# Optimization experiments

Hardware: AMD Instinct MI355X
Metric: run time of the kernel (lower is better)

The kernel has to match this reference:

```python
import jax, jax.numpy as jnp
import numpy as np

B, L, D = 16, 1024, 512
MAX_LEN = 1024  # module hardcodes self.max_len = 1024


def setup_inputs() -> dict:
    key = jax.random.key(0)
    k0, k1, k2, k3, k4 = jax.random.split(key, 5)
    s = 1.0 / np.sqrt(D)
    return {
        "x": jax.random.normal(k0, (B, L, D), jnp.float32),
        "generator": 0.02 * jax.random.normal(k1, (D, 2 * MAX_LEN - 1), jnp.float32),
        "Wq": jax.random.normal(k2, (D, D), jnp.float32) * s,
        "Wv": jax.random.normal(k3, (D, D), jnp.float32) * s,
        "Wc": jax.random.normal(k4, (D, D), jnp.float32) * s,
    }


def reference(x, generator, Wq, Wv, Wc):
    Bc, Lc, Dc = x.shape
    q = x @ Wq.T                      # (B, L, D)
    v = x @ Wv.T                      # (B, L, D)
    # extract_center_window: window of size 2L-1 centered at MAX_LEN-1
    center_full = (generator.shape[-1] + 1) // 2  # == MAX_LEN
    gen = generator[:, center_full - Lc: center_full + Lc - 1]  # (D, 2L-1)
    w = jnp.einsum('bld,di->bli', q, gen)  # (B, L, 2L-1)
    # Toeplitz gather: out[b, l, i] = w[b, l, (L-1) - l + i]
    r = jnp.arange(Lc)
    idx = (Lc - 1) - r[:, None] + r[None, :]  # (L, L)
    w = jnp.take_along_axis(w, idx[None, :, :], axis=-1)  # (B, L, L)
    w = jnp.cumsum(w, axis=1)
    w = jax.nn.relu(w)
    w = jnp.tril(w)
    w = w / (jnp.sum(w, axis=-1, keepdims=True) + 1e-8)
    out = jnp.einsum('bli,bid->bld', w, v)  # (B, L, D)
    return out @ Wc.T
```

## Files before the change

### kernel.cpp

```cpp
#include <hip/hip_runtime.h>
#include <hip/hip_bf16.h>

typedef __attribute__((ext_vector_type(8))) __bf16 bf16x8;
typedef __attribute__((ext_vector_type(4))) __bf16 bf16x4;
typedef __attribute__((ext_vector_type(4))) float  f32x4;

__device__ __forceinline__ void gl_lds16(const __bf16* g, __bf16* l) {
  __builtin_amdgcn_global_load_lds(
      (const __attribute__((address_space(1))) void*)g,
      (__attribute__((address_space(3))) void*)l,
      16, 0, 0);
}

__global__ __launch_bounds__(256) void prep_kernel(
    const float* __restrict__ x, const float* __restrict__ gen,
    const float* __restrict__ Wq, const float* __restrict__ Wv, const float* __restrict__ Wc,
    __bf16* __restrict__ xb, __bf16* __restrict__ genT,
    __bf16* __restrict__ wqT, __bf16* __restrict__ wvT, __bf16* __restrict__ wcb,
    float* __restrict__ gp) {
  __shared__ float S[64][65];
  const int blk = blockIdx.x, tid = threadIdx.x;

  if (blk < 128) {
    const float* in = (blk < 64) ? Wq : Wv;
    __bf16* out = (blk < 64) ? wqT : wvT;
    int t = blk & 63;
    int tx = tid & 63, ty = tid >> 6;
    int d0 = (t >> 3) * 64, e0 = (t & 7) * 64;
#pragma unroll
    for (int i = 0; i < 16; ++i) {
      int di = i * 4 + ty;
      S[di][tx] = in[(long)(d0 + di) * 512 + e0 + tx];
    }
    __syncthreads();
#pragma unroll
    for (int i = 0; i < 16; ++i) {
      int ei = i * 4 + ty;
      out[(long)(e0 + ei) * 512 + d0 + tx] = (__bf16)S[tx][ei];
    }
  } else if (blk < 384) {
    int i = (blk - 128) * 256 + tid;
    float4 v = ((const float4*)Wc)[i];
    bf16x4 o;
    o[0] = (__bf16)v.x; o[1] = (__bf16)v.y; o[2] = (__bf16)v.z; o[3] = (__bf16)v.w;
    *(bf16x4*)(wcb + 4L * i) = o;
  } else if (blk < 2432) {
    int i = blk - 384;
    for (int d = tid; d < 512; d += 256) {
      float v = (i < 2047) ? gen[(long)d * 2047 + i] : 0.f;
      genT[(long)i * 512 + d] = (__bf16)v;
    }
  } else if (blk < 10624) {
    int i = (blk - 2432) * 256 + tid;
    float4 v = ((const float4*)x)[i];
    bf16x4 o;
    o[0] = (__bf16)v.x; o[1] = (__bf16)v.y; o[2] = (__bf16)v.z; o[3] = (__bf16)v.w;
    *(bf16x4*)(xb + 4L * i) = o;
  } else {
    int t = blk - 10624;
    int i = t % 63, c = t / 63;
    int d0 = c * 64, k = tid;
    float a0 = 0.f, a1 = 0.f;
#pragma unroll 8
    for (int u = 0; u < 64; ++u) {
      int d = d0 + u;
      float g = gen[(long)d * 2047 + 992 + i];
      a0 += Wq[(long)d * 512 + k] * g;
      a1 += Wq[(long)d * 512 + k + 256] * g;
    }
    long o = ((long)c * 63 + i) * 512;
    gp[o + k] = a0;
    gp[o + k + 256] = a1;
  }
}

__global__ void g2t_reduce(const float* __restrict__ gp, float* __restrict__ g2t) {
  int idx = blockIdx.x * 256 + threadIdx.x;
  if (idx >= 63 * 512) return;
  float s = 0.f;
#pragma unroll
  for (int c = 0; c < 8; ++c) s += gp[(long)c * 63 * 512 + idx];
  g2t[idx] = s;
}

template <int MODE, bool TRIL = false>
__global__ __launch_bounds__(256) void gemm_bt(
    const __bf16* __restrict__ A, const __bf16* __restrict__ B, void* __restrict__ Cv,
    const float* __restrict__ aux, int N, int K, long sA, long sB, long sC, int sAux) {
  __shared__ __bf16 As[2][128 * 32];
  __shared__ __bf16 Bs[2][128 * 32];
  const int tid = threadIdx.x;
  const int w = tid >> 6, l = tid & 63;
  const int m0 = blockIdx.y * 128;
  const int n0 = blockIdx.x * 128;
  const int bz = blockIdx.z;
  const __bf16* Ab = A + (long)bz * sA;
  const __bf16* Bb = B + (long)bz * sB;

  const int srow = w * 16 + (l >> 2);
  const int scol = (l & 3) * 8;
  const int wr = (w >> 1) * 64, wc = (w & 1) * 64;
  const int fr = l & 15, fk = (l >> 4) * 8;

  f32x4 acc[4][4] = {};

  const int KM = TRIL ? min(K, m0 + 128) : K;
  const int nt = KM >> 5;

  auto STAGE = [&](int t, int p) {
    const int k0 = t << 5;
    gl_lds16(Ab + (long)(m0 + srow) * K + (k0 + scol),      &As[p][(w * 16) * 32]);
    gl_lds16(Ab + (long)(m0 + 64 + srow) * K + (k0 + scol), &As[p][(64 + w * 16) * 32]);
    gl_lds16(Bb + (long)(n0 + srow) * K + (k0 + scol),      &Bs[p][(w * 16) * 32]);
    gl_lds16(Bb + (long)(n0 + 64 + srow) * K + (k0 + scol), &Bs[p][(64 + w * 16) * 32]);
  };

  STAGE(0, 0);
  STAGE(1, 1);

  for (int t = 0; t < nt; ++t) {
    if (t == nt - 1) asm volatile("s_waitcnt vmcnt(0)\ns_barrier" ::: "memory");
    else             asm volatile("s_waitcnt vmcnt(4)\ns_barrier" ::: "memory");
    const int p = t & 1;
    bf16x8 af[4], bg[4];
#pragma unroll
    for (int i = 0; i < 4; ++i) af[i] = *(const bf16x8*)&As[p][(wr + i * 16 + fr) * 32 + fk];
#pragma unroll
    for (int j = 0; j < 4; ++j) bg[j] = *(const bf16x8*)&Bs[p][(wc + j * 16 + fr) * 32 + fk];
    asm volatile("s_waitcnt lgkmcnt(0)\ns_barrier" ::: "memory");
    if (t + 2 < nt) STAGE(t + 2, p);
#pragma unroll
    for (int i = 0; i < 4; ++i)
#pragma unroll
      for (int j = 0; j < 4; ++j)
        acc[i][j] = __builtin_amdgcn_mfma_f32_16x16x32_bf16(af[i], bg[j], acc[i][j], 0, 0, 0);
  }

  const int rbase = m0 + wr + ((l >> 4) << 2);
  const int cbase = n0 + wc + fr;

  if constexpr (MODE == 1) {
    __bf16* C = (__bf16*)Cv + (long)bz * sC;
#pragma unroll
    for (int i = 0; i < 4; ++i)
#pragma unroll
      for (int r = 0; r < 4; ++r) {
        long row = rbase + i * 16 + r;
#pragma unroll
        for (int j = 0; j < 4; ++j) C[row * N + cbase + j * 16] = (__bf16)acc[i][j][r];
      }
  } else {
    float* C = (float*)Cv + (long)bz * sC;
    const float* ax = aux + (long)bz * sAux;
#pragma unroll
    for (int i = 0; i < 4; ++i)
#pragma unroll
      for (int r = 0; r < 4; ++r) {
        long row = rbase + i * 16 + r;
        float sc = 1.f / (ax[row] + 1e-8f);
#pragma unroll
        for (int j = 0; j < 4; ++j) C[row * N + cbase + j * 16] = acc[i][j][r] * sc;
      }
  }
}

__global__ __launch_bounds__(512) void gemm_x(
    const __bf16* __restrict__ A, const __bf16* __restrict__ Bg,
    const __bf16* __restrict__ Pm, __bf16* __restrict__ S, __bf16* __restrict__ vT) {
  __shared__ __bf16 As[2][256 * 32];
  __shared__ __bf16 Bs[2][128 * 32];
  const int tid = threadIdx.x;
  const int w = tid >> 6, l = tid & 63;

  int wgid = blockIdx.x;
  int swz = (wgid & 7) * 112 + (wgid >> 3);
  int y = swz / 14, xt = swz - y * 14;
  const bool band = (xt < 10);
  const int m0 = y * 256;
  const int n0 = band ? (6 - 2 * (y & 3) + xt) * 128 : (xt - 10) * 128;
  const __bf16* Bb = band ? Bg : Pm;
  const int K = 512;

  const int srow = w * 16 + (l >> 2);
  const int scol = (l & 3) * 8;
  const int wr = (w >> 1) * 64;
  const int wc = (w & 1) * 64;
  const int fr = l & 15, fk = (l >> 4) * 8;

  f32x4 acc[4][4] = {};

  auto STAGE = [&](int t, int p) {
    const int k0 = t << 5;
    gl_lds16(A + (long)(m0 + srow) * K + (k0 + scol),        &As[p][(w * 16) * 32]);
    gl_lds16(A + (long)(m0 + 128 + srow) * K + (k0 + scol),  &As[p][(128 + w * 16) * 32]);
    gl_lds16(Bb + (long)(n0 + srow) * K + (k0 + scol),       &Bs[p][(w * 16) * 32]);
  };

  STAGE(0, 0);
  STAGE(1, 1);

  for (int t = 0; t < 16; ++t) {
    if (t == 15) asm volatile("s_waitcnt vmcnt(0)\ns_barrier" ::: "memory");
    else         asm volatile("s_waitcnt vmcnt(3)\ns_barrier" ::: "memory");
    const int p = t & 1;
    bf16x8 af[4], bg[4];
#pragma unroll
    for (int i = 0; i < 4; ++i) af[i] = *(const bf16x8*)&As[p][(wr + i * 16 + fr) * 32 + fk];
#pragma unroll
    for (int j = 0; j < 4; ++j) bg[j] = *(const bf16x8*)&Bs[p][(wc + j * 16 + fr) * 32 + fk];
    asm volatile("s_waitcnt lgkmcnt(0)\ns_barrier" ::: "memory");
    if (t + 2 < 16) STAGE(t + 2, p);
#pragma unroll
    for (int i = 0; i < 4; ++i)
#pragma unroll
      for (int j = 0; j < 4; ++j)
        acc[i][j] = __builtin_amdgcn_mfma_f32_16x16x32_bf16(af[i], bg[j], acc[i][j], 0, 0, 0);
  }

  const int rbase = m0 + wr + ((l >> 4) << 2);
  const int cbase = n0 + wc + fr;

  if (band) {
#pragma unroll
    for (int i = 0; i < 4; ++i)
#pragma unroll
      for (int r = 0; r < 4; ++r) {
        int row = rbase + i * 16 + r;
        int lloc = row & 1023;
#pragma unroll
        for (int j = 0; j < 4; ++j) {
          int jj = cbase + j * 16 - 1023 + lloc;
          if ((unsigned)jj < 1024u)
            S[(long)row * 1024 + jj] = (__bf16)acc[i][j][r];
        }
      }
  } else {
#pragma unroll
    for (int i = 0; i < 4; ++i) {
      int gm = rbase + i * 16;
      int bt = gm >> 10, lloc = gm & 1023;
#pragma unroll
      for (int j = 0; j < 4; ++j) {
        bf16x4 pk;
        pk[0] = (__bf16)acc[i][j][0]; pk[1] = (__bf16)acc[i][j][1];
        pk[2] = (__bf16)acc[i][j][2]; pk[3] = (__bf16)acc[i][j][3];
        *(bf16x4*)&vT[((long)bt * 512 + cbase + j * 16) * 1024 + lloc] = pk;
      }
    }
  }
}

__global__ __launch_bounds__(128) void chunk_sums(const __bf16* __restrict__ S,
                                                  float* __restrict__ csum) {
  int j0 = threadIdx.x * 8;
  int c = blockIdx.x, b = blockIdx.y;
  const __bf16* Sb = S + (long)b * 1024 * 1024;
  float a[8] = {};
  int l0 = c * 16;
  for (int l = l0; l < l0 + 16; ++l) {
    bf16x8 v = *(const bf16x8*)&Sb[(long)l * 1024 + j0];
#pragma unroll
    for (int k = 0; k < 8; ++k) a[k] += (float)v[k];
  }
  long o = ((long)(b * 64 + c) << 10) + j0;
#pragma unroll
  for (int k = 0; k < 8; ++k) csum[o + k] = a[k];
}

__global__ void scan_kernel(float* __restrict__ csum) {
  int idx = blockIdx.x * 256 + threadIdx.x;
  int b = idx >> 10, j = idx & 1023;
  long base = ((long)b * 64 << 10) + j;
  float s = 0.f;
  for (int c = 0; c < 64; ++c) {
    long o = base + ((long)c << 10);
    float t = csum[o];
    csum[o] = s;
    s += t;
  }
}

__global__ __launch_bounds__(128) void cumsum_relu(const __bf16* __restrict__ S,
                                                   const float* __restrict__ csum,
                                                   __bf16* __restrict__ wrelu,
                                                   float* __restrict__ rowsum) {
  int j0 = threadIdx.x * 8;
  int c = blockIdx.x, b = blockIdx.y;
  float run[8];
  long co = ((long)(b * 64 + c) << 10) + j0;
#pragma unroll
  for (int k = 0; k < 8; ++k) run[k] = csum[co + k];
  const __bf16* Sb = S + (long)b * 1024 * 1024;
  __bf16* wr = wrelu + (long)b * 1024 * 1024;
  int l0 = c * 16;
  for (int l = l0; l < l0 + 16; ++l) {
    bf16x8 v = *(const bf16x8*)&Sb[(long)l * 1024 + j0];
    bf16x8 o;
    float rs = 0.f;
#pragma unroll
    for (int k = 0; k < 8; ++k) {
      run[k] += (float)v[k];
      float val = (j0 + k <= l) ? fmaxf(run[k], 0.f) : 0.f;
      o[k] = (__bf16)val;
      rs += val;
    }
    *(bf16x8*)&wr[(long)l * 1024 + j0] = o;
#pragma unroll
    for (int off = 32; off; off >>= 1) rs += __shfl_down(rs, off);
    if ((threadIdx.x & 63) == 0 && rs != 0.f) atomicAdd(&rowsum[b * 1024 + l], rs);
  }
}

__global__ __launch_bounds__(256) void small_dots(
    const float* __restrict__ x, const float* __restrict__ g2t, float* __restrict__ S) {
  int gid = blockIdx.x * 4 + (threadIdx.x >> 6);
  int lane = threadIdx.x & 63;
  int b = gid >> 10, rem = gid & 1023, m = rem >> 5, j = rem & 31;
  const float4* xr = (const float4*)(x + ((long)b * 1024 + m) * 512);
  const float4* gr = (const float4*)(g2t + (long)(31 - m + j) * 512);
  float4 a0 = xr[lane * 2], a1 = xr[lane * 2 + 1];
  float4 c0 = gr[lane * 2], c1 = gr[lane * 2 + 1];
  float s = a0.x * c0.x + a0.y * c0.y + a0.z * c0.z + a0.w * c0.w
          + a1.x * c1.x + a1.y * c1.y + a1.z * c1.z + a1.w * c1.w;
#pragma unroll
  for (int off = 32; off; off >>= 1) s += __shfl_down(s, off);
  if (lane == 0) S[gid] = s;
}

__global__ __launch_bounds__(1024) void small_scan(
    const float* __restrict__ Sg, __bf16* __restrict__ wrelu, float* __restrict__ rowsum) {
  int b = blockIdx.x, tid = threadIdx.x;
  __shared__ float S[32][33];
  int m = tid >> 5, j = tid & 31;
  S[m][j] = Sg[b * 1024 + tid];
  __syncthreads();
  if (tid < 32) {
    float run = 0.f;
    for (int mm = 0; mm < 32; ++mm) { run += S[mm][tid]; S[mm][tid] = run; }
  }
  __syncthreads();
  float v = (j <= m) ? fmaxf(S[m][j], 0.f) : 0.f;
  wrelu[((long)b * 1024 + m) * 1024 + j] = (__bf16)v;
  float rs = v;
#pragma unroll
  for (int off = 16; off; off >>= 1) rs += __shfl_down(rs, off, 32);
  if (j == 0) rowsum[b * 1024 + m] = rs;
}

extern "C" void kernel_launch(void* const* d_in, const int* in_sizes, int n_in,
                              void* d_out, int out_size, void* d_ws, size_t ws_size,
                              hipStream_t stream) {
  const float* x   = (const float*)d_in[0];
  const float* gen = (const float*)d_in[1];
  const float* Wq  = (const float*)d_in[2];
  const float* Wv  = (const float*)d_in[3];
  const float* Wc  = (const float*)d_in[4];

  char* ws = (char*)d_ws;
  __bf16* xb    = (__bf16*)(ws + 0L);
  __bf16* vT    = (__bf16*)(ws + 33554432L);
  __bf16* Smat  = (__bf16*)(ws + 67108864L);
  __bf16* wrelu = (__bf16*)(ws + 134217728L);
  __bf16* genT  = (__bf16*)(ws + 167772160L);
  __bf16* wqT   = (__bf16*)(ws + 169869312L);
  __bf16* wvT   = (__bf16*)(ws + 170393600L);
  __bf16* wcb   = (__bf16*)(ws + 170917888L);
  float*  g2t   = (float*)(ws + 171442176L);
  float*  csum  = (float*)(ws + 16777216L);
  float*  rsum  = (float*)(ws + 16777216L + 4194304L);
  float*  Sbuf  = (float*)(ws + 16777216L + 4259840L);
  __bf16* Pmat  = (__bf16*)(ws + 50331648L);
  __bf16* Bg    = (__bf16*)(ws + 51380224L);
  float*  gp    = (float*)(ws + 58720256L);

  prep_kernel<<<11128, 256, 0, stream>>>(x, gen, Wq, Wv, Wc, xb, genT, wqT, wvT, wcb, gp);
  g2t_reduce<<<126, 256, 0, stream>>>(gp, g2t);

  gemm_bt<1><<<dim3(4, 4, 1), 256, 0, stream>>>(wcb, wvT, Pmat, nullptr, 512, 512, 0, 0, 0, 0);
  gemm_bt<1><<<dim3(4, 16, 1), 256, 0, stream>>>(genT, wqT, Bg, nullptr, 512, 512, 0, 0, 0, 0);

  gemm_x<<<896, 512, 0, stream>>>(xb, Bg, Pmat, Smat, vT);

  chunk_sums<<<dim3(64, 16), 128, 0, stream>>>(Smat, csum);
  scan_kernel<<<64, 256, 0, stream>>>(csum);
  hipMemsetAsync(rsum, 0, 16 * 1024 * 4, stream);
  cumsum_relu<<<dim3(64, 16), 128, 0, stream>>>(Smat, csum, wrelu, rsum);

  small_dots<<<4096, 256, 0, stream>>>(x, g2t, Sbuf);
  small_scan<<<16, 1024, 0, stream>>>(Sbuf, wrelu, rsum);

  gemm_bt<4, true><<<dim3(4, 8, 16), 256, 0, stream>>>(wrelu, vT, d_out, rsum, 512, 1024,
                                                 1024L * 1024, 512L * 1024, 512L * 1024, 1024);
}
```

Baseline: 158.1 us.

## Triple-buffer GEMM pipelines, merge weight-fold GEMMs, drop memset and dead-tile writes

Moves the shared GEMM mainloop and gemm_x from double to triple LDS buffering with three tiles in flight, to hide more global-load latency. The two small weight-folding GEMMs become one 80-block launch, and the rowsum memset moves into chunk_sums, saving launches. cumsum_relu now skips writing wrelu tiles above the 128-block diagonal, which the tril-limited output GEMM never reads. Triple buffering raises LDS use per block, which may lower occupancy.

```diff
diff --git a/kernel.cpp b/kernel.cpp
--- a/kernel.cpp
+++ b/kernel.cpp
@@ -83,29 +83,15 @@
   g2t[idx] = s;
 }
 
-template <int MODE, bool TRIL = false>
-__global__ __launch_bounds__(256) void gemm_bt(
-    const __bf16* __restrict__ A, const __bf16* __restrict__ B, void* __restrict__ Cv,
-    const float* __restrict__ aux, int N, int K, long sA, long sB, long sC, int sAux) {
-  __shared__ __bf16 As[2][128 * 32];
-  __shared__ __bf16 Bs[2][128 * 32];
+__device__ __forceinline__ void gemm128_body(
+    const __bf16* __restrict__ Ab, const __bf16* __restrict__ Bb,
+    __bf16 (*As)[128 * 32], __bf16 (*Bs)[128 * 32],
+    int m0, int n0, int K, int nt, f32x4 (&acc)[4][4]) {
   const int tid = threadIdx.x;
   const int w = tid >> 6, l = tid & 63;
-  const int m0 = blockIdx.y * 128;
-  const int n0 = blockIdx.x * 128;
-  const int bz = blockIdx.z;
-  const __bf16* Ab = A + (long)bz * sA;
-  const __bf16* Bb = B + (long)bz * sB;
-
-  const int srow = w * 16 + (l >> 2);
-  const int scol = (l & 3) * 8;
+  const int srow = w * 16 + (l >> 2), scol = (l & 3) * 8;
   const int wr = (w >> 1) * 64, wc = (w & 1) * 64;
   const int fr = l & 15, fk = (l >> 4) * 8;
-
-  f32x4 acc[4][4] = {};
-
-  const int KM = TRIL ? min(K, m0 + 128) : K;
-  const int nt = KM >> 5;
 
   auto STAGE = [&](int t, int p) {
     const int k0 = t << 5;
@@ -114,61 +100,92 @@
     gl_lds16(Bb + (long)(n0 + srow) * K + (k0 + scol),      &Bs[p][(w * 16) * 32]);
     gl_lds16(Bb + (long)(n0 + 64 + srow) * K + (k0 + scol), &Bs[p][(64 + w * 16) * 32]);
   };
-
   STAGE(0, 0);
-  STAGE(1, 1);
-
+  if (nt > 1) STAGE(1, 1);
+  if (nt > 2) STAGE(2, 2);
+  int p = 0;
   for (int t = 0; t < nt; ++t) {
-    if (t == nt - 1) asm volatile("s_waitcnt vmcnt(0)\ns_barrier" ::: "memory");
-    else             asm volatile("s_waitcnt vmcnt(4)\ns_barrier" ::: "memory");
-    const int p = t & 1;
+    const int ahead = nt - 1 - t;
+    if (ahead >= 2)      asm volatile("s_waitcnt vmcnt(8)\ns_barrier" ::: "memory");
+    else if (ahead == 1) asm volatile("s_waitcnt vmcnt(4)\ns_barrier" ::: "memory");
+    else                 asm volatile("s_waitcnt vmcnt(0)\ns_barrier" ::: "memory");
     bf16x8 af[4], bg[4];
 #pragma unroll
     for (int i = 0; i < 4; ++i) af[i] = *(const bf16x8*)&As[p][(wr + i * 16 + fr) * 32 + fk];
 #pragma unroll
     for (int j = 0; j < 4; ++j) bg[j] = *(const bf16x8*)&Bs[p][(wc + j * 16 + fr) * 32 + fk];
     asm volatile("s_waitcnt lgkmcnt(0)\ns_barrier" ::: "memory");
-    if (t + 2 < nt) STAGE(t + 2, p);
+    if (t + 3 < nt) STAGE(t + 3, p);
 #pragma unroll
     for (int i = 0; i < 4; ++i)
 #pragma unroll
       for (int j = 0; j < 4; ++j)
         acc[i][j] = __builtin_amdgcn_mfma_f32_16x16x32_bf16(af[i], bg[j], acc[i][j], 0, 0, 0);
-  }
-
-  const int rbase = m0 + wr + ((l >> 4) << 2);
-  const int cbase = n0 + wc + fr;
-
-  if constexpr (MODE == 1) {
-    __bf16* C = (__bf16*)Cv + (long)bz * sC;
-#pragma unroll
-    for (int i = 0; i < 4; ++i)
-#pragma unroll
-      for (int r = 0; r < 4; ++r) {
-        long row = rbase + i * 16 + r;
-#pragma unroll
-        for (int j = 0; j < 4; ++j) C[row * N + cbase + j * 16] = (__bf16)acc[i][j][r];
-      }
-  } else {
-    float* C = (float*)Cv + (long)bz * sC;
-    const float* ax = aux + (long)bz * sAux;
-#pragma unroll
-    for (int i = 0; i < 4; ++i)
-#pragma unroll
-      for (int r = 0; r < 4; ++r) {
-        long row = rbase + i * 16 + r;
-        float sc = 1.f / (ax[row] + 1e-8f);
-#pragma unroll
-        for (int j = 0; j < 4; ++j) C[row * N + cbase + j * 16] = acc[i][j][r] * sc;
-      }
-  }
+    p = (p == 2) ? 0 : p + 1;
+  }
+}
+
+__global__ __launch_bounds__(256) void gemm_fold(
+    const __bf16* __restrict__ A1, const __bf16* __restrict__ B1, __bf16* __restrict__ C1,
+    const __bf16* __restrict__ A2, const __bf16* __restrict__ B2, __bf16* __restrict__ C2) {
+  __shared__ __bf16 As[3][128 * 32];
+  __shared__ __bf16 Bs[3][128 * 32];
+  const int b = blockIdx.x;
+  const __bf16 *Ab, *Bb; __bf16* C; int m0, n0;
+  if (b < 16) { Ab = A1; Bb = B1; C = C1; m0 = (b >> 2) * 128; n0 = (b & 3) * 128; }
+  else { int t = b - 16; Ab = A2; Bb = B2; C = C2; m0 = (t >> 2) * 128; n0 = (t & 3) * 128; }
+
+  f32x4 acc[4][4] = {};
+  gemm128_body(Ab, Bb, As, Bs, m0, n0, 512, 16, acc);
+
+  const int l = threadIdx.x & 63, w = threadIdx.x >> 6;
+  const int rbase = m0 + (w >> 1) * 64 + ((l >> 4) << 2);
+  const int cbase = n0 + (w & 1) * 64 + (l & 15);
+#pragma unroll
+  for (int i = 0; i < 4; ++i)
+#pragma unroll
+    for (int r = 0; r < 4; ++r) {
+      long row = rbase + i * 16 + r;
+#pragma unroll
+      for (int j = 0; j < 4; ++j) C[row * 512 + cbase + j * 16] = (__bf16)acc[i][j][r];
+    }
+}
+
+__global__ __launch_bounds__(256) void gemm_out(
+    const __bf16* __restrict__ A, const __bf16* __restrict__ B, float* __restrict__ Cv,
+    const float* __restrict__ aux) {
+  __shared__ __bf16 As[3][128 * 32];
+  __shared__ __bf16 Bs[3][128 * 32];
+  const int m0 = blockIdx.y * 128, n0 = blockIdx.x * 128, bz = blockIdx.z;
+  const int K = 1024;
+  const __bf16* Ab = A + (long)bz * 1024 * 1024;
+  const __bf16* Bb = B + (long)bz * 512 * 1024;
+  const int nt = (m0 + 128) >> 5;
+
+  f32x4 acc[4][4] = {};
+  gemm128_body(Ab, Bb, As, Bs, m0, n0, K, nt, acc);
+
+  const int l = threadIdx.x & 63, w = threadIdx.x >> 6;
+  const int rbase = m0 + (w >> 1) * 64 + ((l >> 4) << 2);
+  const int cbase = n0 + (w & 1) * 64 + (l & 15);
+  float* C = Cv + (long)bz * 512 * 1024;
+  const float* ax = aux + bz * 1024;
+#pragma unroll
+  for (int i = 0; i < 4; ++i)
+#pragma unroll
+    for (int r = 0; r < 4; ++r) {
+      long row = rbase + i * 16 + r;
+      float sc = 1.f / (ax[row] + 1e-8f);
+#pragma unroll
+      for (int j = 0; j < 4; ++j) C[row * 512 + cbase + j * 16] = acc[i][j][r] * sc;
+    }
 }
 
 __global__ __launch_bounds__(512) void gemm_x(
     const __bf16* __restrict__ A, const __bf16* __restrict__ Bg,
     const __bf16* __restrict__ Pm, __bf16* __restrict__ S, __bf16* __restrict__ vT) {
-  __shared__ __bf16 As[2][256 * 32];
-  __shared__ __bf16 Bs[2][128 * 32];
+  __shared__ __bf16 As[3][256 * 32];
+  __shared__ __bf16 Bs[3][128 * 32];
   const int tid = threadIdx.x;
   const int w = tid >> 6, l = tid & 63;
 
@@ -198,23 +215,27 @@
 
   STAGE(0, 0);
   STAGE(1, 1);
-
+  STAGE(2, 2);
+
+  int p = 0;
   for (int t = 0; t < 16; ++t) {
-    if (t == 15) asm volatile("s_waitcnt vmcnt(0)\ns_barrier" ::: "memory");
-    else         asm volatile("s_waitcnt vmcnt(3)\ns_barrier" ::: "memory");
-    const int p = t & 1;
+    const int ahead = 15 - t;
+    if (ahead >= 2)      asm volatile("s_waitcnt vmcnt(6)\ns_barrier" ::: "memory");
+    else if (ahead == 1) asm volatile("s_waitcnt vmcnt(3)\ns_barrier" ::: "memory");
+    else                 asm volatile("s_waitcnt vmcnt(0)\ns_barrier" ::: "memory");
     bf16x8 af[4], bg[4];
 #pragma unroll
     for (int i = 0; i < 4; ++i) af[i] = *(const bf16x8*)&As[p][(wr + i * 16 + fr) * 32 + fk];
 #pragma unroll
     for (int j = 0; j < 4; ++j) bg[j] = *(const bf16x8*)&Bs[p][(wc + j * 16 + fr) * 32 + fk];
     asm volatile("s_waitcnt lgkmcnt(0)\ns_barrier" ::: "memory");
-    if (t + 2 < 16) STAGE(t + 2, p);
+    if (t + 3 < 16) STAGE(t + 3, p);
 #pragma unroll
     for (int i = 0; i < 4; ++i)
 #pragma unroll
       for (int j = 0; j < 4; ++j)
         acc[i][j] = __builtin_amdgcn_mfma_f32_16x16x32_bf16(af[i], bg[j], acc[i][j], 0, 0, 0);
+    p = (p == 2) ? 0 : p + 1;
   }
 
   const int rbase = m0 + wr + ((l >> 4) << 2);
@@ -251,9 +272,11 @@
 }
 
 __global__ __launch_bounds__(128) void chunk_sums(const __bf16* __restrict__ S,
-                                                  float* __restrict__ csum) {
+                                                  float* __restrict__ csum,
+                                                  float* __restrict__ rowsum) {
   int j0 = threadIdx.x * 8;
   int c = blockIdx.x, b = blockIdx.y;
+  if (c < 8) rowsum[b * 1024 + c * 128 + threadIdx.x] = 0.f;
   const __bf16* Sb = S + (long)b * 1024 * 1024;
   float a[8] = {};
   int l0 = c * 16;
@@ -304,7 +327,8 @@
       o[k] = (__bf16)val;
       rs += val;
     }
-    *(bf16x8*)&wr[(long)l * 1024 + j0] = o;
+    if (j0 < (((l >> 7) + 1) << 7))
+      *(bf16x8*)&wr[(long)l * 1024 + j0] = o;
 #pragma unroll
     for (int off = 32; off; off >>= 1) rs += __shfl_down(rs, off);
     if ((threadIdx.x & 63) == 0 && rs != 0.f) atomicAdd(&rowsum[b * 1024 + l], rs);
@@ -376,19 +400,16 @@
   prep_kernel<<<11128, 256, 0, stream>>>(x, gen, Wq, Wv, Wc, xb, genT, wqT, wvT, wcb, gp);
   g2t_reduce<<<126, 256, 0, stream>>>(gp, g2t);
 
-  gemm_bt<1><<<dim3(4, 4, 1), 256, 0, stream>>>(wcb, wvT, Pmat, nullptr, 512, 512, 0, 0, 0, 0);
-  gemm_bt<1><<<dim3(4, 16, 1), 256, 0, stream>>>(genT, wqT, Bg, nullptr, 512, 512, 0, 0, 0, 0);
+  gemm_fold<<<80, 256, 0, stream>>>(wcb, wvT, Pmat, genT, wqT, Bg);
 
   gemm_x<<<896, 512, 0, stream>>>(xb, Bg, Pmat, Smat, vT);
 
-  chunk_sums<<<dim3(64, 16), 128, 0, stream>>>(Smat, csum);
+  chunk_sums<<<dim3(64, 16), 128, 0, stream>>>(Smat, csum, rsum);
   scan_kernel<<<64, 256, 0, stream>>>(csum);
-  hipMemsetAsync(rsum, 0, 16 * 1024 * 4, stream);
   cumsum_relu<<<dim3(64, 16), 128, 0, stream>>>(Smat, csum, wrelu, rsum);
 
   small_dots<<<4096, 256, 0, stream>>>(x, g2t, Sbuf);
   small_scan<<<16, 1024, 0, stream>>>(Sbuf, wrelu, rsum);
 
-  gemm_bt<4, true><<<dim3(4, 8, 16), 256, 0, stream>>>(wrelu, vT, d_out, rsum, 512, 1024,
-                                                 1024L * 1024, 512L * 1024, 512L * 1024, 1024);
-}
+  gemm_out<<<dim3(4, 8, 16), 256, 0, stream>>>(wrelu, vT, (float*)d_out, rsum);
+}
```

New measurement: 143.9 us. 9.0% less time.
